# Kernel tuning notes

Measured on AMD Instinct MI355X. Metric: run time of the kernel, lower is better.

Reference implementation:

```python
import jax, jax.numpy as jnp
import numpy as np

N_ITER = 2
M = 0.0
AFF_SOFTMAX = 1.0
BIG = 1e16  # finite sentinel for invalid neighbors (CUDA kernel uses inf)


def _ssn(x, s):
    B, C, H, W = x.shape
    nh, nw = H // s, W // s
    S = nh * nw
    N = H * W
    # append_grid: concat (row, col) coordinate channels scaled by M/stoken
    ii, jj = jnp.meshgrid(jnp.arange(H), jnp.arange(W), indexing='ij')
    grid = jnp.stack([ii, jj], 0).astype(x.dtype) * (M / s)  # (2,H,W)
    xg = jnp.concatenate([x, jnp.broadcast_to(grid[None], (B, 2, H, W))], 1)
    C2 = C + 2
    # adaptive_avg_pool2d with exact divisibility == block mean
    cent = xg.reshape(B, C2, nh, s, nw, s).mean(axis=(3, 5)).reshape(B, C2, S)
    # nearest-neighbor init label map (exact divisibility => i//s)
    ly = jnp.broadcast_to((jnp.arange(H) // s)[:, None], (H, W)).reshape(-1)
    lx = jnp.broadcast_to((jnp.arange(W) // s)[None, :], (H, W)).reshape(-1)
    dy = jnp.repeat(jnp.arange(-1, 2), 3)  # 9-neighborhood offsets
    dx = jnp.tile(jnp.arange(-1, 2), 3)
    ny = ly[None, :] + dy[:, None]  # (9,N)
    nx = lx[None, :] + dx[:, None]
    valid = (ny >= 0) & (ny < nh) & (nx >= 0) & (nx < nw)
    nidx = jnp.clip(ny, 0, nh - 1) * nw + jnp.clip(nx, 0, nw - 1)  # (9,N)
    pix = jnp.arange(N)
    bidx = jnp.arange(B)[:, None, None]
    px = xg.reshape(B, C2, N)
    abs_aff = None
    for k in range(N_ITER):
        cg = cent[:, :, nidx]                              # (B,C2,9,N) gather
        dist = ((px[:, :, None, :] - cg) ** 2).sum(1)      # (B,9,N)
        dist = jnp.where(valid[None], dist, BIG)
        aff = jax.nn.softmax(-AFF_SOFTMAX * dist, axis=1)  # softmax over 9 nbrs
        aff = jnp.where(valid[None], aff, 0.0)
        # sparse_coo_tensor(...).to_dense() == scatter-add into (B,S,N)
        abs_aff = jnp.zeros((B, S, N), x.dtype).at[bidx, nidx[None], pix].add(aff)
        if k < N_ITER - 1:
            num = jnp.einsum('bsn,bcn->bcs', abs_aff, px)  # weighted bmm
            den = abs_aff.sum(2)[:, None] + 1e-16
            cent = num / den
    return abs_aff, S


def setup_inputs() -> dict:
    key = jax.random.key(0)
    x = jax.random.normal(key, (4, 32, 256, 256), dtype=jnp.float32)
    return {"x": x, "stoken_size": 16}


def reference(x, stoken_size):
    return _ssn(x, int(stoken_size))
```

## Files before the change

### kernel.cpp

```cpp
#include <hip/hip_runtime.h>

#define B_  4
#define C_  32
#define H_  256
#define W_  256
#define N_  65536
#define NH_ 16
#define S_  256
#define PADP 260
#define PSTR 304

__device__ __forceinline__ float wave_sum(float v) {
    v += __shfl_down(v, 32);
    v += __shfl_down(v, 16);
    v += __shfl_down(v, 8);
    v += __shfl_down(v, 4);
    v += __shfl_down(v, 2);
    v += __shfl_down(v, 1);
    return v;
}

__device__ __forceinline__ void stage_tile(const float* __restrict__ x,
                                           int b, int sy, int sx, int t,
                                           float (*xsh)[PADP]) {
    const float* base = x + (size_t)b * C_ * N_ + (sy * 16) * W_ + sx * 16;
    #pragma unroll
    for (int i = 0; i < 8; ++i) {
        const int idx = i * 256 + t;
        const int c = idx >> 6, p4 = idx & 63;
        const int py = p4 >> 2, px4 = (p4 & 3) * 4;
        const float4 v = *(const float4*)(base + (size_t)c * N_ + py * W_ + px4);
        *(float4*)&xsh[c][p4 * 4] = v;
    }
}

__device__ __forceinline__ void compute_aff(const float xv[C_], const float (*cl)[C_],
                                            int sy, int sx, float aff[9]) {
    float dist[9];
    #pragma unroll
    for (int k = 0; k < 9; ++k) {
        const int ny = sy + k / 3 - 1, nx = sx + k % 3 - 1;
        const bool valid = (ny >= 0) & (ny < NH_) & (nx >= 0) & (nx < NH_);
        float d = 0.f;
        #pragma unroll
        for (int c4 = 0; c4 < C_ / 4; ++c4) {
            const float4 cv = *(const float4*)&cl[k][c4 * 4];
            const float d0 = xv[c4 * 4 + 0] - cv.x;
            const float d1 = xv[c4 * 4 + 1] - cv.y;
            const float d2 = xv[c4 * 4 + 2] - cv.z;
            const float d3 = xv[c4 * 4 + 3] - cv.w;
            d += d0 * d0 + d1 * d1 + d2 * d2 + d3 * d3;
        }
        dist[k] = valid ? d : 1e30f;
    }
    float mind = dist[0];
    #pragma unroll
    for (int k = 1; k < 9; ++k) mind = fminf(mind, dist[k]);
    float sum = 0.f;
    #pragma unroll
    for (int k = 0; k < 9; ++k) {
        const float e = (dist[k] < 1e29f) ? __expf(mind - dist[k]) : 0.f;
        aff[k] = e;
        sum += e;
    }
    const float inv = 1.f / sum;
    #pragma unroll
    for (int k = 0; k < 9; ++k) aff[k] *= inv;
}

__device__ __forceinline__ void load_cl(const float* __restrict__ cent,
                                        int b, int sy, int sx, int t,
                                        float (*cl)[C_]) {
    {
        const int k = t >> 5, c = t & 31;
        const int ny = sy + k / 3 - 1, nx = sx + k % 3 - 1;
        const bool valid = (ny >= 0) & (ny < NH_) & (nx >= 0) & (nx < NH_);
        cl[k][c] = valid ? cent[(size_t)(b * S_ + ny * NH_ + nx) * C_ + c] : 0.f;
    }
    if (t < 32) {
        const int ny = sy + 1, nx = sx + 1;
        const bool valid = (ny < NH_) & (nx < NH_);
        cl[8][t] = valid ? cent[(size_t)(b * S_ + ny * NH_ + nx) * C_ + t] : 0.f;
    }
}

__global__ __launch_bounds__(256) void k_cent0(const float* __restrict__ x,
                                               float* __restrict__ cent0) {
    const int blk = blockIdx.x;
    const int b = blk >> 8, s = blk & 255;
    const int sy = s >> 4, sx = s & 15;
    const int t = threadIdx.x;
    const int w = t >> 6, lane = t & 63;
    const int py = sy * 16 + (t >> 4), pxc = sx * 16 + (t & 15);
    const float* xb = x + (size_t)b * C_ * N_ + py * W_ + pxc;
    __shared__ float acc[C_][4];
    #pragma unroll
    for (int c = 0; c < C_; ++c) {
        const float v = wave_sum(xb[c * N_]);
        if (lane == 0) acc[c][w] = v;
    }
    __syncthreads();
    if (t < C_)
        cent0[(size_t)blk * C_ + t] =
            (acc[t][0] + acc[t][1] + acc[t][2] + acc[t][3]) * (1.0f / 256.0f);
}

__global__ __launch_bounds__(256) void k_part(const float* __restrict__ x,
                                              const float* __restrict__ cent0,
                                              float* __restrict__ part) {
    const int blk = blockIdx.x;
    const int b = blk >> 8, s = blk & 255;
    const int sy = s >> 4, sx = s & 15;
    const int t = threadIdx.x;
    const int w = t >> 6, lane = t & 63;
    __shared__ float cl[9][C_];
    __shared__ float xsh[C_][PADP];
    __shared__ float affs[9][PADP];
    __shared__ float lden[4][9];
    load_cl(cent0, b, sy, sx, t, cl);
    stage_tile(x, b, sy, sx, t, xsh);
    __syncthreads();
    float xv[C_];
    #pragma unroll
    for (int c = 0; c < C_; ++c) xv[c] = xsh[c][t];
    float aff[9];
    compute_aff(xv, cl, sy, sx, aff);
    #pragma unroll
    for (int k = 0; k < 9; ++k) {
        affs[k][t] = aff[k];
        const float v = wave_sum(aff[k]);
        if (lane == 0) lden[w][k] = v;
    }
    __syncthreads();
    {
        const int k = t >> 5, c = t & 31;
        float acc2 = 0.f;
        #pragma unroll 4
        for (int p = 0; p < 256; p += 4) {
            const float4 a = *(const float4*)&affs[k][p];
            const float4 xc = *(const float4*)&xsh[c][p];
            acc2 += a.x * xc.x + a.y * xc.y + a.z * xc.z + a.w * xc.w;
        }
        part[(size_t)blk * PSTR + t] = acc2;
    }
    if (t < 32) {
        float acc2 = 0.f;
        #pragma unroll 4
        for (int p = 0; p < 256; p += 4) {
            const float4 a = *(const float4*)&affs[8][p];
            const float4 xc = *(const float4*)&xsh[t][p];
            acc2 += a.x * xc.x + a.y * xc.y + a.z * xc.z + a.w * xc.w;
        }
        part[(size_t)blk * PSTR + 256 + t] = acc2;
    }
    if (t < 9)
        part[(size_t)blk * PSTR + 288 + t] =
            lden[0][t] + lden[1][t] + lden[2][t] + lden[3][t];
}

__global__ __launch_bounds__(256) void k_cent1(const float* __restrict__ part,
                                               float* __restrict__ cent1) {
    const int g = blockIdx.x * 256 + threadIdx.x;
    const int c = g & 31, s = (g >> 5) & 255, b = g >> 13;
    const int sy = s >> 4, sx = s & 15;
    float num = 0.f, den = 0.f;
    #pragma unroll
    for (int k = 0; k < 9; ++k) {
        const int syp = sy - (k / 3 - 1), sxp = sx - (k % 3 - 1);
        if ((syp >= 0) & (syp < NH_) & (sxp >= 0) & (sxp < NH_)) {
            const size_t base = (size_t)(b * S_ + syp * NH_ + sxp) * PSTR;
            num += part[base + k * 32 + c];
            den += part[base + 288 + k];
        }
    }
    cent1[g] = num / (den + 1e-16f);
}

__global__ __launch_bounds__(256) void k_aff9(const float* __restrict__ x,
                                              const float* __restrict__ cent1,
                                              float* __restrict__ aff9) {
    const int blk = blockIdx.x;
    const int b = blk >> 8, s = blk & 255;
    const int sy = s >> 4, sx = s & 15;
    const int t = threadIdx.x;
    __shared__ float cl[9][C_];
    __shared__ float xsh[C_][PADP];
    __shared__ float affs[9][PADP];
    load_cl(cent1, b, sy, sx, t, cl);
    stage_tile(x, b, sy, sx, t, xsh);
    __syncthreads();
    float xv[C_];
    #pragma unroll
    for (int c = 0; c < C_; ++c) xv[c] = xsh[c][t];
    float aff[9];
    compute_aff(xv, cl, sy, sx, aff);
    #pragma unroll
    for (int k = 0; k < 9; ++k) affs[k][t] = aff[k];
    __syncthreads();
    #pragma unroll
    for (int i = 0; i < 3; ++i) {
        const int idx = i * 256 + t;
        if (idx < 576) {
            const int k = idx >> 6, j4 = idx & 63;
            const int py = j4 >> 2, px4 = (j4 & 3) * 4;
            const float4 v = *(const float4*)&affs[k][j4 * 4];
            const int n = (sy * 16 + py) * W_ + sx * 16 + px4;
            *(float4*)(aff9 + ((size_t)(b * 9 + k) << 16) + n) = v;
        }
    }
}

__global__ __launch_bounds__(256) void k_write(const float* __restrict__ aff9,
                                               float* __restrict__ out) {
    const int t = threadIdx.x;
    const int bs = blockIdx.x >> 3;
    const int b = bs >> 8, s = bs & 255;
    const int sdy = (s >> 4) + 1, sdx = (s & 15) + 1;
    const int qb = (blockIdx.x & 7) * 2048 + t;
    const float* plane = aff9 + ((size_t)b * 9 << 16);
    float4* outp = (float4*)out + ((size_t)bs << 14);
    #pragma unroll
    for (int i = 0; i < 8; ++i) {
        const int q = qb + i * 256;
        const int ly = q >> 10;
        const int lx = (q >> 2) & 15;
        const int dy = sdy - ly, dx = sdx - lx;
        float4 v = make_float4(0.f, 0.f, 0.f, 0.f);
        if (((unsigned)dy <= 2u) & ((unsigned)dx <= 2u))
            v = *(const float4*)(plane + ((size_t)(dy * 3 + dx) << 16) + (q << 2));
        outp[q] = v;
    }
    if ((blockIdx.x | t) == 0) out[(size_t)B_ * S_ * N_] = 256.0f;
}

extern "C" void kernel_launch(void* const* d_in, const int* in_sizes, int n_in,
                              void* d_out, int out_size, void* d_ws, size_t ws_size,
                              hipStream_t stream) {
    const float* x = (const float*)d_in[0];
    float* ws = (float*)d_ws;
    float* cent0 = ws;
    float* part  = ws + 32768;
    float* cent1 = ws + 32768 + 1024 * PSTR;
    float* aff9  = ws + 32768 + 1024 * PSTR + 32768;
    float* out   = (float*)d_out;

    hipLaunchKernelGGL(k_cent0, dim3(B_ * S_), dim3(256), 0, stream, x, cent0);
    hipLaunchKernelGGL(k_part,  dim3(B_ * S_), dim3(256), 0, stream, x, cent0, part);
    hipLaunchKernelGGL(k_cent1, dim3(B_ * S_ * C_ / 256), dim3(256), 0, stream, part, cent1);
    hipLaunchKernelGGL(k_aff9,  dim3(B_ * S_), dim3(256), 0, stream, x, cent1, aff9);
    hipLaunchKernelGGL(k_write, dim3(B_ * S_ * 8), dim3(256), 0, stream, aff9, out);
}
```

Baseline: 361.4 us.

## Fuse cent1 and output-write kernels into part/aff9, zero-fill output early

The k_cent1 and k_write kernels are removed. Centroid recomputation is folded into k_aff9, which now gathers partials directly, and k_aff9 scatters the nonzero affinity tiles straight into the dense output. Zero-filling the large dense output is split between k_part and k_aff9, so it runs alongside compute instead of in a separate pass. k_cent0 is also vectorised to float4 loads with no shared-memory reduction. This removes the aff9 intermediate round trip and two launches, at the cost of redundant per-block centroid gathers and scattered writes.

```diff
diff --git a/kernel.cpp b/kernel.cpp
--- a/kernel.cpp
+++ b/kernel.cpp
@@ -2,7 +2,6 @@
 
 #define B_  4
 #define C_  32
-#define H_  256
 #define W_  256
 #define N_  65536
 #define NH_ 16
@@ -28,8 +27,7 @@
     for (int i = 0; i < 8; ++i) {
         const int idx = i * 256 + t;
         const int c = idx >> 6, p4 = idx & 63;
-        const int py = p4 >> 2, px4 = (p4 & 3) * 4;
-        const float4 v = *(const float4*)(base + (size_t)c * N_ + py * W_ + px4);
+        const float4 v = *(const float4*)(base + (size_t)c * N_ + (p4 >> 2) * W_ + (p4 & 3) * 4);
         *(float4*)&xsh[c][p4 * 4] = v;
     }
 }
@@ -68,22 +66,6 @@
     for (int k = 0; k < 9; ++k) aff[k] *= inv;
 }
 
-__device__ __forceinline__ void load_cl(const float* __restrict__ cent,
-                                        int b, int sy, int sx, int t,
-                                        float (*cl)[C_]) {
-    {
-        const int k = t >> 5, c = t & 31;
-        const int ny = sy + k / 3 - 1, nx = sx + k % 3 - 1;
-        const bool valid = (ny >= 0) & (ny < NH_) & (nx >= 0) & (nx < NH_);
-        cl[k][c] = valid ? cent[(size_t)(b * S_ + ny * NH_ + nx) * C_ + c] : 0.f;
-    }
-    if (t < 32) {
-        const int ny = sy + 1, nx = sx + 1;
-        const bool valid = (ny < NH_) & (nx < NH_);
-        cl[8][t] = valid ? cent[(size_t)(b * S_ + ny * NH_ + nx) * C_ + t] : 0.f;
-    }
-}
-
 __global__ __launch_bounds__(256) void k_cent0(const float* __restrict__ x,
                                                float* __restrict__ cent0) {
     const int blk = blockIdx.x;
@@ -91,23 +73,20 @@
     const int sy = s >> 4, sx = s & 15;
     const int t = threadIdx.x;
     const int w = t >> 6, lane = t & 63;
-    const int py = sy * 16 + (t >> 4), pxc = sx * 16 + (t & 15);
-    const float* xb = x + (size_t)b * C_ * N_ + py * W_ + pxc;
-    __shared__ float acc[C_][4];
-    #pragma unroll
-    for (int c = 0; c < C_; ++c) {
-        const float v = wave_sum(xb[c * N_]);
-        if (lane == 0) acc[c][w] = v;
-    }
-    __syncthreads();
-    if (t < C_)
-        cent0[(size_t)blk * C_ + t] =
-            (acc[t][0] + acc[t][1] + acc[t][2] + acc[t][3]) * (1.0f / 256.0f);
+    const float* base = x + (size_t)b * C_ * N_ + (sy * 16) * W_ + sx * 16;
+    #pragma unroll
+    for (int i = 0; i < 8; ++i) {
+        const int c = i * 4 + w;
+        const float4 v = *(const float4*)(base + (size_t)c * N_ + (lane >> 2) * W_ + (lane & 3) * 4);
+        const float sm = wave_sum(v.x + v.y + v.z + v.w);
+        if (lane == 0) cent0[(size_t)blk * C_ + c] = sm * (1.0f / 256.0f);
+    }
 }
 
 __global__ __launch_bounds__(256) void k_part(const float* __restrict__ x,
                                               const float* __restrict__ cent0,
-                                              float* __restrict__ part) {
+                                              float* __restrict__ part,
+                                              float* __restrict__ out) {
     const int blk = blockIdx.x;
     const int b = blk >> 8, s = blk & 255;
     const int sy = s >> 4, sx = s & 15;
@@ -117,8 +96,30 @@
     __shared__ float xsh[C_][PADP];
     __shared__ float affs[9][PADP];
     __shared__ float lden[4][9];
-    load_cl(cent0, b, sy, sx, t, cl);
+    {
+        const int k = t >> 5, c = t & 31;
+        const int ny = sy + k / 3 - 1, nx = sx + k % 3 - 1;
+        const bool valid = (ny >= 0) & (ny < NH_) & (nx >= 0) & (nx < NH_);
+        cl[k][c] = valid ? cent0[(size_t)(b * S_ + ny * NH_ + nx) * C_ + c] : 0.f;
+    }
+    if (t < 32) {
+        const int ny = sy + 1, nx = sx + 1;
+        const bool valid = (ny < NH_) & (nx < NH_);
+        cl[8][t] = valid ? cent0[(size_t)(b * S_ + ny * NH_ + nx) * C_ + t] : 0.f;
+    }
     stage_tile(x, b, sy, sx, t, xsh);
+    {
+        const float4 z = make_float4(0.f, 0.f, 0.f, 0.f);
+        float4* plane = (float4*)out + ((size_t)blk << 14);
+        #pragma unroll
+        for (int i = 0; i < 32; ++i) {
+            const int q = i * 256 + t;
+            const int ty = q >> 10;
+            const int tx = (q >> 2) & 15;
+            if (((unsigned)(ty - sy + 1) > 2u) | ((unsigned)(tx - sx + 1) > 2u))
+                plane[q] = z;
+        }
+    }
     __syncthreads();
     float xv[C_];
     #pragma unroll
@@ -134,51 +135,48 @@
     __syncthreads();
     {
         const int k = t >> 5, c = t & 31;
-        float acc2 = 0.f;
+        float acc = 0.f;
         #pragma unroll 4
         for (int p = 0; p < 256; p += 4) {
             const float4 a = *(const float4*)&affs[k][p];
             const float4 xc = *(const float4*)&xsh[c][p];
-            acc2 += a.x * xc.x + a.y * xc.y + a.z * xc.z + a.w * xc.w;
-        }
-        part[(size_t)blk * PSTR + t] = acc2;
+            acc += a.x * xc.x + a.y * xc.y + a.z * xc.z + a.w * xc.w;
+        }
+        part[(size_t)blk * PSTR + t] = acc;
     }
     if (t < 32) {
-        float acc2 = 0.f;
+        float acc = 0.f;
         #pragma unroll 4
         for (int p = 0; p < 256; p += 4) {
             const float4 a = *(const float4*)&affs[8][p];
             const float4 xc = *(const float4*)&xsh[t][p];
-            acc2 += a.x * xc.x + a.y * xc.y + a.z * xc.z + a.w * xc.w;
-        }
-        part[(size_t)blk * PSTR + 256 + t] = acc2;
+            acc += a.x * xc.x + a.y * xc.y + a.z * xc.z + a.w * xc.w;
+        }
+        part[(size_t)blk * PSTR + 256 + t] = acc;
     }
     if (t < 9)
         part[(size_t)blk * PSTR + 288 + t] =
             lden[0][t] + lden[1][t] + lden[2][t] + lden[3][t];
 }
 
-__global__ __launch_bounds__(256) void k_cent1(const float* __restrict__ part,
-                                               float* __restrict__ cent1) {
-    const int g = blockIdx.x * 256 + threadIdx.x;
-    const int c = g & 31, s = (g >> 5) & 255, b = g >> 13;
-    const int sy = s >> 4, sx = s & 15;
+__device__ __forceinline__ float gather_cent1(const float* __restrict__ part,
+                                              int b, int ny, int nx, int c) {
     float num = 0.f, den = 0.f;
     #pragma unroll
-    for (int k = 0; k < 9; ++k) {
-        const int syp = sy - (k / 3 - 1), sxp = sx - (k % 3 - 1);
+    for (int k2 = 0; k2 < 9; ++k2) {
+        const int syp = ny - (k2 / 3 - 1), sxp = nx - (k2 % 3 - 1);
         if ((syp >= 0) & (syp < NH_) & (sxp >= 0) & (sxp < NH_)) {
             const size_t base = (size_t)(b * S_ + syp * NH_ + sxp) * PSTR;
-            num += part[base + k * 32 + c];
-            den += part[base + 288 + k];
-        }
-    }
-    cent1[g] = num / (den + 1e-16f);
+            num += part[base + k2 * 32 + c];
+            den += part[base + 288 + k2];
+        }
+    }
+    return num / (den + 1e-16f);
 }
 
 __global__ __launch_bounds__(256) void k_aff9(const float* __restrict__ x,
-                                              const float* __restrict__ cent1,
-                                              float* __restrict__ aff9) {
+                                              const float* __restrict__ part,
+                                              float* __restrict__ out) {
     const int blk = blockIdx.x;
     const int b = blk >> 8, s = blk & 255;
     const int sy = s >> 4, sx = s & 15;
@@ -186,8 +184,30 @@
     __shared__ float cl[9][C_];
     __shared__ float xsh[C_][PADP];
     __shared__ float affs[9][PADP];
-    load_cl(cent1, b, sy, sx, t, cl);
+    {
+        const int k = t >> 5, c = t & 31;
+        const int ny = sy + k / 3 - 1, nx = sx + k % 3 - 1;
+        const bool valid = (ny >= 0) & (ny < NH_) & (nx >= 0) & (nx < NH_);
+        cl[k][c] = valid ? gather_cent1(part, b, ny, nx, c) : 0.f;
+    }
+    if (t < 32) {
+        const int ny = sy + 1, nx = sx + 1;
+        const bool valid = (ny < NH_) & (nx < NH_);
+        cl[8][t] = valid ? gather_cent1(part, b, ny, nx, t) : 0.f;
+    }
     stage_tile(x, b, sy, sx, t, xsh);
+    {
+        const float4 z = make_float4(0.f, 0.f, 0.f, 0.f);
+        float4* plane = (float4*)out + ((size_t)blk << 14);
+        #pragma unroll
+        for (int i = 32; i < 64; ++i) {
+            const int q = i * 256 + t;
+            const int ty = q >> 10;
+            const int tx = (q >> 2) & 15;
+            if (((unsigned)(ty - sy + 1) > 2u) | ((unsigned)(tx - sx + 1) > 2u))
+                plane[q] = z;
+        }
+    }
     __syncthreads();
     float xv[C_];
     #pragma unroll
@@ -202,35 +222,15 @@
         const int idx = i * 256 + t;
         if (idx < 576) {
             const int k = idx >> 6, j4 = idx & 63;
-            const int py = j4 >> 2, px4 = (j4 & 3) * 4;
-            const float4 v = *(const float4*)&affs[k][j4 * 4];
-            const int n = (sy * 16 + py) * W_ + sx * 16 + px4;
-            *(float4*)(aff9 + ((size_t)(b * 9 + k) << 16) + n) = v;
-        }
-    }
-}
-
-__global__ __launch_bounds__(256) void k_write(const float* __restrict__ aff9,
-                                               float* __restrict__ out) {
-    const int t = threadIdx.x;
-    const int bs = blockIdx.x >> 3;
-    const int b = bs >> 8, s = bs & 255;
-    const int sdy = (s >> 4) + 1, sdx = (s & 15) + 1;
-    const int qb = (blockIdx.x & 7) * 2048 + t;
-    const float* plane = aff9 + ((size_t)b * 9 << 16);
-    float4* outp = (float4*)out + ((size_t)bs << 14);
-    #pragma unroll
-    for (int i = 0; i < 8; ++i) {
-        const int q = qb + i * 256;
-        const int ly = q >> 10;
-        const int lx = (q >> 2) & 15;
-        const int dy = sdy - ly, dx = sdx - lx;
-        float4 v = make_float4(0.f, 0.f, 0.f, 0.f);
-        if (((unsigned)dy <= 2u) & ((unsigned)dx <= 2u))
-            v = *(const float4*)(plane + ((size_t)(dy * 3 + dx) << 16) + (q << 2));
-        outp[q] = v;
-    }
-    if ((blockIdx.x | t) == 0) out[(size_t)B_ * S_ * N_] = 256.0f;
+            const int ny = sy + k / 3 - 1, nx = sx + k % 3 - 1;
+            if ((ny >= 0) & (ny < NH_) & (nx >= 0) & (nx < NH_)) {
+                const float4 v = *(const float4*)&affs[k][j4 * 4];
+                const int gq = (sy * 16 + (j4 >> 2)) * 64 + sx * 4 + (j4 & 3);
+                ((float4*)out)[((size_t)(b * S_ + ny * NH_ + nx) << 14) + gq] = v;
+            }
+        }
+    }
+    if ((blk | t) == 0) out[(size_t)B_ * S_ * N_] = 256.0f;
 }
 
 extern "C" void kernel_launch(void* const* d_in, const int* in_sizes, int n_in,
@@ -240,13 +240,9 @@
     float* ws = (float*)d_ws;
     float* cent0 = ws;
     float* part  = ws + 32768;
-    float* cent1 = ws + 32768 + 1024 * PSTR;
-    float* aff9  = ws + 32768 + 1024 * PSTR + 32768;
     float* out   = (float*)d_out;
 
     hipLaunchKernelGGL(k_cent0, dim3(B_ * S_), dim3(256), 0, stream, x, cent0);
-    hipLaunchKernelGGL(k_part,  dim3(B_ * S_), dim3(256), 0, stream, x, cent0, part);
-    hipLaunchKernelGGL(k_cent1, dim3(B_ * S_ * C_ / 256), dim3(256), 0, stream, part, cent1);
-    hipLaunchKernelGGL(k_aff9,  dim3(B_ * S_), dim3(256), 0, stream, x, cent1, aff9);
-    hipLaunchKernelGGL(k_write, dim3(B_ * S_ * 8), dim3(256), 0, stream, aff9, out);
-}
+    hipLaunchKernelGGL(k_part,  dim3(B_ * S_), dim3(256), 0, stream, x, cent0, part, out);
+    hipLaunchKernelGGL(k_aff9,  dim3(B_ * S_), dim3(256), 0, stream, x, part, out);
+}
```

After: 320.8 us. 11.3% less time.
